# Kernel tuning notes

Measured on AMD Instinct MI355X. Metric: run time of the kernel, lower is better.

The kernel has to match this reference:

```python
import jax, jax.numpy as jnp
import numpy as np

N_NODES = 50000
N_EDGES = 625000
IN_DIM = 128
OUT_DIM = 128


def setup_inputs() -> dict:
    key = jax.random.key(0)
    ks = jax.random.split(key, 8)
    feats = jax.random.normal(ks[0], (N_NODES, IN_DIM), dtype=jnp.float32)
    src = jax.random.randint(ks[1], (N_EDGES,), 0, N_NODES, dtype=jnp.int64)
    dst = jax.random.randint(ks[2], (N_EDGES,), 0, N_NODES, dtype=jnp.int64)
    # nn.Linear default init: U(-1/sqrt(fan_in), 1/sqrt(fan_in))
    bf = 1.0 / np.sqrt(IN_DIM)
    W_f = jax.random.uniform(ks[3], (OUT_DIM, IN_DIM), jnp.float32, -bf, bf)
    b_f = jax.random.uniform(ks[4], (OUT_DIM,), jnp.float32, -bf, bf)
    bp = 1.0 / np.sqrt(OUT_DIM)
    W_phy = jax.random.uniform(ks[5], (OUT_DIM, OUT_DIM), jnp.float32, -bp, bp)
    b_phy = jax.random.uniform(ks[6], (OUT_DIM,), jnp.float32, -bp, bp)
    eps = jnp.zeros((1,), dtype=jnp.float32)  # init_eps = 0
    return {"feats": feats, "src": src, "dst": dst, "W_f": W_f, "b_f": b_f,
            "W_phy": W_phy, "b_phy": b_phy, "eps": eps}


def reference(feats, src, dst, W_f, b_f, W_phy, b_phy, eps):
    # mlp_f (num_mlps=1): linear + relu
    h = jax.nn.relu(feats @ W_f.T + b_f)              # [N, out_dim]
    # update_all(copy_u('h'), sum): sum messages h[src] at dst
    n = jax.ops.segment_sum(h[src], dst, num_segments=N_NODES)  # [N, out_dim]
    # faithful to source: h = 1 + eps * h + n
    h = 1.0 + eps * h + n
    # mlp_phy (num_mlps=1): linear + relu
    h = jax.nn.relu(h @ W_phy.T + b_phy)
    return h
```

## Files before the change

kernel.cpp:

```cpp
#include <hip/hip_runtime.h>

#define N_NODES 50000
#define N_EDGES 625000
#define DIM 128
#define RCAP 16
#define OCAP 64

typedef __bf16 bf16x8 __attribute__((ext_vector_type(8)));
typedef __bf16 bf16x4 __attribute__((ext_vector_type(4)));
typedef __bf16 bf16x2 __attribute__((ext_vector_type(2)));
typedef float f32x4 __attribute__((ext_vector_type(4)));

__device__ __forceinline__ float bflo(unsigned u) { return __uint_as_float(u << 16); }
__device__ __forceinline__ float bfhi(unsigned u) { return __uint_as_float(u & 0xffff0000u); }

__global__ __launch_bounds__(512) void gemm1_fill_k(
    const float* __restrict__ A_f32,
    const float* __restrict__ W,
    const float* __restrict__ bias,
    __bf16* __restrict__ out_bf16,
    const int* __restrict__ src,
    const int* __restrict__ dst,
    int* __restrict__ cnt9,
    int* __restrict__ bucket,
    int* __restrict__ obucket,
    const float* __restrict__ W_phy,
    __bf16* __restrict__ Wb,
    int gemm_blocks)
{
    const int t = threadIdx.x;

    if ((int)blockIdx.x >= gemm_blocks) {
        if ((int)blockIdx.x == gemm_blocks) {
            if (t < 16) {
                bf16x8 z = {};
                *(bf16x8*)&out_bf16[(size_t)N_NODES * DIM + t * 8] = z;
            }
            for (int i = t; i < 4096; i += 512) {
                float4 f = ((const float4*)W_phy)[i];
                bf16x4 pk = { (__bf16)f.x, (__bf16)f.y, (__bf16)f.z, (__bf16)f.w };
                *(bf16x4*)&Wb[i * 4] = pk;
            }
        }
        int xcd;
        asm volatile("s_getreg_b32 %0, hwreg(HW_REG_XCC_ID)" : "=s"(xcd));
        xcd &= 7;
        const int cb = xcd * N_NODES;

        int idx = ((int)blockIdx.x - gemm_blocks) * 512 + t;
        if (idx < N_EDGES / 8) {
            int4 sa = ((const int4*)src)[idx * 2];
            int4 sb = ((const int4*)src)[idx * 2 + 1];
            int4 da = ((const int4*)dst)[idx * 2];
            int4 db = ((const int4*)dst)[idx * 2 + 1];
            int p0 = atomicAdd(&cnt9[cb + da.x], 1);
            int p1 = atomicAdd(&cnt9[cb + da.y], 1);
            int p2 = atomicAdd(&cnt9[cb + da.z], 1);
            int p3 = atomicAdd(&cnt9[cb + da.w], 1);
            int p4 = atomicAdd(&cnt9[cb + db.x], 1);
            int p5 = atomicAdd(&cnt9[cb + db.y], 1);
            int p6 = atomicAdd(&cnt9[cb + db.z], 1);
            int p7 = atomicAdd(&cnt9[cb + db.w], 1);
            if (p0 < RCAP) bucket[((cb + da.x) << 4) + p0] = sa.x;
            else { int q = atomicAdd(&cnt9[8 * N_NODES + da.x], 1); obucket[(da.x << 6) + q] = sa.x; }
            if (p1 < RCAP) bucket[((cb + da.y) << 4) + p1] = sa.y;
            else { int q = atomicAdd(&cnt9[8 * N_NODES + da.y], 1); obucket[(da.y << 6) + q] = sa.y; }
            if (p2 < RCAP) bucket[((cb + da.z) << 4) + p2] = sa.z;
            else { int q = atomicAdd(&cnt9[8 * N_NODES + da.z], 1); obucket[(da.z << 6) + q] = sa.z; }
            if (p3 < RCAP) bucket[((cb + da.w) << 4) + p3] = sa.w;
            else { int q = atomicAdd(&cnt9[8 * N_NODES + da.w], 1); obucket[(da.w << 6) + q] = sa.w; }
            if (p4 < RCAP) bucket[((cb + db.x) << 4) + p4] = sb.x;
            else { int q = atomicAdd(&cnt9[8 * N_NODES + db.x], 1); obucket[(db.x << 6) + q] = sb.x; }
            if (p5 < RCAP) bucket[((cb + db.y) << 4) + p5] = sb.y;
            else { int q = atomicAdd(&cnt9[8 * N_NODES + db.y], 1); obucket[(db.y << 6) + q] = sb.y; }
            if (p6 < RCAP) bucket[((cb + db.z) << 4) + p6] = sb.z;
            else { int q = atomicAdd(&cnt9[8 * N_NODES + db.z], 1); obucket[(db.z << 6) + q] = sb.z; }
            if (p7 < RCAP) bucket[((cb + db.w) << 4) + p7] = sb.w;
            else { int q = atomicAdd(&cnt9[8 * N_NODES + db.w], 1); obucket[(db.w << 6) + q] = sb.w; }
        }
        return;
    }

    __shared__ __align__(16) __bf16 w_lds[128 * 136];

    for (int i = t; i < 4096; i += 512) {
        float4 f = ((const float4*)W)[i];
        int n = i >> 5;
        int k = (i & 31) << 2;
        bf16x4 pk = { (__bf16)f.x, (__bf16)f.y, (__bf16)f.z, (__bf16)f.w };
        *(bf16x4*)&w_lds[n * 136 + k] = pk;
    }
    __syncthreads();

    const int wave = t >> 6;
    const int lane = t & 63;
    const int q = lane >> 4;
    const int mr = lane & 15;

    const int m0 = blockIdx.x * 128 + wave * 16;
    int arow = m0 + mr;
    if (arow >= N_NODES) arow = N_NODES - 1;

    f32x4 acc[8] = {};

#pragma unroll
    for (int ks = 0; ks < 4; ++ks) {
        const int k0 = ks * 32 + q * 8;
        const float4* ap = (const float4*)&A_f32[(size_t)arow * DIM + k0];
        float4 a0 = ap[0], a1 = ap[1];
        bf16x8 af;
        af[0] = (__bf16)a0.x; af[1] = (__bf16)a0.y;
        af[2] = (__bf16)a0.z; af[3] = (__bf16)a0.w;
        af[4] = (__bf16)a1.x; af[5] = (__bf16)a1.y;
        af[6] = (__bf16)a1.z; af[7] = (__bf16)a1.w;
#pragma unroll
        for (int nt = 0; nt < 8; ++nt) {
            bf16x8 bfr = *(const bf16x8*)&w_lds[(nt * 16 + mr) * 136 + k0];
            acc[nt] = __builtin_amdgcn_mfma_f32_16x16x32_bf16(af, bfr, acc[nt], 0, 0, 0);
        }
    }

    __syncthreads();
    float* lds_f = (float*)w_lds;
    const int nb = blockIdx.x * 128;

#pragma unroll
    for (int half = 0; half < 2; ++half) {
        if ((wave >> 2) == half) {
            int lw = wave & 3;
#pragma unroll
            for (int nt = 0; nt < 8; ++nt)
#pragma unroll
                for (int r = 0; r < 4; ++r)
                    lds_f[(lw * 16 + q * 4 + r) * 132 + nt * 16 + mr] = acc[nt][r];
        }
        __syncthreads();
        for (int i = t; i < 2048; i += 512) {
            int lr = i >> 5;
            int cg = (i & 31) << 2;
            int grow = nb + half * 64 + lr;
            if (grow < N_NODES) {
                float4 v = *(const float4*)&lds_f[lr * 132 + cg];
                float4 b4 = *(const float4*)&bias[cg];
                bf16x4 o;
                o[0] = (__bf16)fmaxf(v.x + b4.x, 0.f);
                o[1] = (__bf16)fmaxf(v.y + b4.y, 0.f);
                o[2] = (__bf16)fmaxf(v.z + b4.z, 0.f);
                o[3] = (__bf16)fmaxf(v.w + b4.w, 0.f);
                *(bf16x4*)&out_bf16[(size_t)grow * DIM + cg] = o;
            }
        }
        __syncthreads();
    }
}

__global__ __launch_bounds__(512, 4) void agg_gemm2_k(
    const __bf16* __restrict__ h,
    const int* __restrict__ cnt9,
    const int* __restrict__ bucket,
    const int* __restrict__ obucket,
    const float* __restrict__ eps_p,
    const __bf16* __restrict__ Wb,
    const float* __restrict__ bias,
    float* __restrict__ out)
{
    __shared__ __align__(16) __bf16 lds[2 * 128 * 136];
    __shared__ __align__(16) int widx_all[8][200];
    __bf16* const w_lds = lds;
    __bf16* const a_lds = lds + 128 * 136;

    const int t = threadIdx.x;

    for (int i = t; i < 2048; i += 512) {
        int n = i >> 4;
        int kk = (i & 15) << 3;
        bf16x8 v = *(const bf16x8*)&Wb[n * DIM + kk];
        *(bf16x8*)&w_lds[n * 136 + kk] = v;
    }

    const int wave = t >> 6;
    const int lane = t & 63;
    const int ch = lane << 1;
    const int xq = lane >> 4;
    const int sj = lane & 15;
    const int rowbase = __builtin_amdgcn_readfirstlane(blockIdx.x * 128 + wave * 16);
    const float eps = eps_p[0];
    int* const widx = widx_all[wave];

    int ndv[2], cAv[2], cBv[2], rAv[2], rBv[2], ocv[2];
    unsigned svv[2];
    auto nload = [&](int sl, int ii) {
        const int node = rowbase + ii;
        const int nd = (node < N_NODES) ? node : (N_NODES - 1);
        ndv[sl] = nd;
        int ca = cnt9[xq * N_NODES + nd];
        int cb = cnt9[(xq + 4) * N_NODES + nd];
        cAv[sl] = (ca < RCAP) ? ca : RCAP;
        cBv[sl] = (cb < RCAP) ? cb : RCAP;
        rAv[sl] = bucket[((xq * N_NODES + nd) << 4) + sj];
        rBv[sl] = bucket[(((xq + 4) * N_NODES + nd) << 4) + sj];
        ocv[sl] = cnt9[8 * N_NODES + nd];
        svv[sl] = *(const unsigned*)&h[(size_t)nd * DIM + ch];
    };
    nload(0, 0);

#pragma unroll
    for (int i = 0; i < 16; ++i) {
        if (i < 15) nload((i + 1) & 1, i + 1);
        const int sl = i & 1;
        const int nd = ndv[sl];

        const unsigned long long mA = __ballot(sj < cAv[sl]);
        const unsigned long long mB = __ballot(sj < cBv[sl]);
        const unsigned long long below = (1ull << lane) - 1ull;
        const int tA = __popcll(mA);
        int deg = tA + __popcll(mB);
        if (sj < cAv[sl]) widx[__popcll(mA & below)] = rAv[sl];
        if (sj < cBv[sl]) widx[tA + __popcll(mB & below)] = rBv[sl];
        const int oc = ocv[sl];
        if (oc > 0) {
            if (lane < oc) widx[deg + lane] = obucket[(nd << 6) + lane];
            deg += oc;
        }
        if (lane < 8) widx[deg + lane] = N_NODES;

        float ax = 0.f, ay = 0.f;
        for (int e = 0; e < deg; e += 8) {
            int4 w0 = *(const int4*)&widx[e];
            int4 w1 = *(const int4*)&widx[e + 4];
            unsigned v0 = *(const unsigned*)&h[(size_t)w0.x * DIM + ch];
            unsigned v1 = *(const unsigned*)&h[(size_t)w0.y * DIM + ch];
            unsigned v2 = *(const unsigned*)&h[(size_t)w0.z * DIM + ch];
            unsigned v3 = *(const unsigned*)&h[(size_t)w0.w * DIM + ch];
            unsigned v4 = *(const unsigned*)&h[(size_t)w1.x * DIM + ch];
            unsigned v5 = *(const unsigned*)&h[(size_t)w1.y * DIM + ch];
            unsigned v6 = *(const unsigned*)&h[(size_t)w1.z * DIM + ch];
            unsigned v7 = *(const unsigned*)&h[(size_t)w1.w * DIM + ch];
            ax += (bflo(v0) + bflo(v1)) + (bflo(v2) + bflo(v3))
                + (bflo(v4) + bflo(v5)) + (bflo(v6) + bflo(v7));
            ay += (bfhi(v0) + bfhi(v1)) + (bfhi(v2) + bfhi(v3))
                + (bfhi(v4) + bfhi(v5)) + (bfhi(v6) + bfhi(v7));
        }
        ax = 1.0f + eps * bflo(svv[sl]) + ax;
        ay = 1.0f + eps * bfhi(svv[sl]) + ay;
        bf16x2 o; o[0] = (__bf16)ax; o[1] = (__bf16)ay;
        *(bf16x2*)&a_lds[(wave * 16 + i) * 136 + ch] = o;
    }

    __syncthreads();

    const int q = lane >> 4;
    const int mr = lane & 15;

    f32x4 acc[8] = {};

#pragma unroll
    for (int ks = 0; ks < 4; ++ks) {
        const int k0 = ks * 32 + q * 8;
        bf16x8 af = *(const bf16x8*)&a_lds[(wave * 16 + mr) * 136 + k0];
#pragma unroll
        for (int nt = 0; nt < 8; ++nt) {
            bf16x8 bfr = *(const bf16x8*)&w_lds[(nt * 16 + mr) * 136 + k0];
            acc[nt] = __builtin_amdgcn_mfma_f32_16x16x32_bf16(af, bfr, acc[nt], 0, 0, 0);
        }
    }

    __syncthreads();
    float* lds_f = (float*)lds;
    const int nb = blockIdx.x * 128;

#pragma unroll
    for (int half = 0; half < 2; ++half) {
        if ((wave >> 2) == half) {
            int lw = wave & 3;
#pragma unroll
            for (int nt = 0; nt < 8; ++nt)
#pragma unroll
                for (int r = 0; r < 4; ++r)
                    lds_f[(lw * 16 + q * 4 + r) * 132 + nt * 16 + mr] = acc[nt][r];
        }
        __syncthreads();
        for (int i2 = t; i2 < 2048; i2 += 512) {
            int lr = i2 >> 5;
            int cg = (i2 & 31) << 2;
            int grow = nb + half * 64 + lr;
            if (grow < N_NODES) {
                float4 v = *(const float4*)&lds_f[lr * 132 + cg];
                float4 b4 = *(const float4*)&bias[cg];
                v.x = fmaxf(v.x + b4.x, 0.f);
                v.y = fmaxf(v.y + b4.y, 0.f);
                v.z = fmaxf(v.z + b4.z, 0.f);
                v.w = fmaxf(v.w + b4.w, 0.f);
                *(float4*)&out[(size_t)grow * DIM + cg] = v;
            }
        }
        __syncthreads();
    }
}

extern "C" void kernel_launch(void* const* d_in, const int* in_sizes, int n_in,
                              void* d_out, int out_size, void* d_ws, size_t ws_size,
                              hipStream_t stream) {
    const float* feats = (const float*)d_in[0];
    const int*   src   = (const int*)d_in[1];
    const int*   dst   = (const int*)d_in[2];
    const float* W_f   = (const float*)d_in[3];
    const float* b_f   = (const float*)d_in[4];
    const float* W_phy = (const float*)d_in[5];
    const float* b_phy = (const float*)d_in[6];
    const float* eps   = (const float*)d_in[7];
    float* out = (float*)d_out;

    const size_t HN = (size_t)(N_NODES + 1) * DIM;
    __bf16* h    = (__bf16*)d_ws;
    int* bucket  = (int*)(h + HN);
    int* obucket = bucket + (size_t)8 * N_NODES * RCAP;
    int* cnt9    = obucket + (size_t)N_NODES * OCAP;
    __bf16* Wb   = (__bf16*)(cnt9 + (size_t)9 * N_NODES);

    const int gblocks = (N_NODES + 127) / 128;
    const int fblocks = (N_EDGES / 8 + 511) / 512;

    hipMemsetAsync(cnt9, 0, (size_t)9 * N_NODES * sizeof(int), stream);

    gemm1_fill_k<<<gblocks + fblocks, 512, 0, stream>>>(
        feats, W_f, b_f, h, src, dst, cnt9, bucket, obucket, W_phy, Wb, gblocks);

    agg_gemm2_k<<<gblocks, 512, 0, stream>>>(
        h, cnt9, bucket, obucket, eps, Wb, b_phy, out);
}
```

Before: 154.7 us.

## Split fused GEMM1/fill kernel and store bucket source indices as 16-bit

The fused kernel that ran the first GEMM and the edge bucketing as different block ranges is split into two separate launches, gemm1_k and fill_k. The bucket array now stores source node ids as unsigned short instead of int, which halves its footprint and the bytes written and gathered for bucket entries. The 16-bit ids fit only because N_NODES is below 65536. Splitting the kernel gives up the concurrent execution of the compute-bound GEMM and the atomic-bound fill, and adds a launch.

```diff
diff --git a/kernel.cpp b/kernel.cpp
--- a/kernel.cpp
+++ b/kernel.cpp
@@ -14,73 +14,75 @@
 __device__ __forceinline__ float bflo(unsigned u) { return __uint_as_float(u << 16); }
 __device__ __forceinline__ float bfhi(unsigned u) { return __uint_as_float(u & 0xffff0000u); }
 
-__global__ __launch_bounds__(512) void gemm1_fill_k(
+__global__ __launch_bounds__(512) void fill_k(
+    const int* __restrict__ src,
+    const int* __restrict__ dst,
+    int* __restrict__ cnt9,
+    unsigned short* __restrict__ bucket,
+    int* __restrict__ obucket,
+    const float* __restrict__ W_phy,
+    __bf16* __restrict__ Wb,
+    __bf16* __restrict__ out_bf16)
+{
+    const int t = threadIdx.x;
+
+    if (blockIdx.x == 0) {
+        if (t < 16) {
+            bf16x8 z = {};
+            *(bf16x8*)&out_bf16[(size_t)N_NODES * DIM + t * 8] = z;
+        }
+        for (int i = t; i < 4096; i += 512) {
+            float4 f = ((const float4*)W_phy)[i];
+            bf16x4 pk = { (__bf16)f.x, (__bf16)f.y, (__bf16)f.z, (__bf16)f.w };
+            *(bf16x4*)&Wb[i * 4] = pk;
+        }
+    }
+
+    int xcd;
+    asm volatile("s_getreg_b32 %0, hwreg(HW_REG_XCC_ID)" : "=s"(xcd));
+    xcd &= 7;
+    const int cb = xcd * N_NODES;
+
+    const int idx = (int)blockIdx.x * 512 + t;
+    if (idx < N_EDGES / 8) {
+        int4 sa = ((const int4*)src)[idx * 2];
+        int4 sb = ((const int4*)src)[idx * 2 + 1];
+        int4 da = ((const int4*)dst)[idx * 2];
+        int4 db = ((const int4*)dst)[idx * 2 + 1];
+        int p0 = atomicAdd(&cnt9[cb + da.x], 1);
+        int p1 = atomicAdd(&cnt9[cb + da.y], 1);
+        int p2 = atomicAdd(&cnt9[cb + da.z], 1);
+        int p3 = atomicAdd(&cnt9[cb + da.w], 1);
+        int p4 = atomicAdd(&cnt9[cb + db.x], 1);
+        int p5 = atomicAdd(&cnt9[cb + db.y], 1);
+        int p6 = atomicAdd(&cnt9[cb + db.z], 1);
+        int p7 = atomicAdd(&cnt9[cb + db.w], 1);
+        if (p0 < RCAP) bucket[((cb + da.x) << 4) + p0] = (unsigned short)sa.x;
+        else { int q = atomicAdd(&cnt9[8 * N_NODES + da.x], 1); obucket[(da.x << 6) + q] = sa.x; }
+        if (p1 < RCAP) bucket[((cb + da.y) << 4) + p1] = (unsigned short)sa.y;
+        else { int q = atomicAdd(&cnt9[8 * N_NODES + da.y], 1); obucket[(da.y << 6) + q] = sa.y; }
+        if (p2 < RCAP) bucket[((cb + da.z) << 4) + p2] = (unsigned short)sa.z;
+        else { int q = atomicAdd(&cnt9[8 * N_NODES + da.z], 1); obucket[(da.z << 6) + q] = sa.z; }
+        if (p3 < RCAP) bucket[((cb + da.w) << 4) + p3] = (unsigned short)sa.w;
+        else { int q = atomicAdd(&cnt9[8 * N_NODES + da.w], 1); obucket[(da.w << 6) + q] = sa.w; }
+        if (p4 < RCAP) bucket[((cb + db.x) << 4) + p4] = (unsigned short)sb.x;
+        else { int q = atomicAdd(&cnt9[8 * N_NODES + db.x], 1); obucket[(db.x << 6) + q] = sb.x; }
+        if (p5 < RCAP) bucket[((cb + db.y) << 4) + p5] = (unsigned short)sb.y;
+        else { int q = atomicAdd(&cnt9[8 * N_NODES + db.y], 1); obucket[(db.y << 6) + q] = sb.y; }
+        if (p6 < RCAP) bucket[((cb + db.z) << 4) + p6] = (unsigned short)sb.z;
+        else { int q = atomicAdd(&cnt9[8 * N_NODES + db.z], 1); obucket[(db.z << 6) + q] = sb.z; }
+        if (p7 < RCAP) bucket[((cb + db.w) << 4) + p7] = (unsigned short)sb.w;
+        else { int q = atomicAdd(&cnt9[8 * N_NODES + db.w], 1); obucket[(db.w << 6) + q] = sb.w; }
+    }
+}
+
+__global__ __launch_bounds__(512) void gemm1_k(
     const float* __restrict__ A_f32,
     const float* __restrict__ W,
     const float* __restrict__ bias,
-    __bf16* __restrict__ out_bf16,
-    const int* __restrict__ src,
-    const int* __restrict__ dst,
-    int* __restrict__ cnt9,
-    int* __restrict__ bucket,
-    int* __restrict__ obucket,
-    const float* __restrict__ W_phy,
-    __bf16* __restrict__ Wb,
-    int gemm_blocks)
+    __bf16* __restrict__ out_bf16)
 {
     const int t = threadIdx.x;
-
-    if ((int)blockIdx.x >= gemm_blocks) {
-        if ((int)blockIdx.x == gemm_blocks) {
-            if (t < 16) {
-                bf16x8 z = {};
-                *(bf16x8*)&out_bf16[(size_t)N_NODES * DIM + t * 8] = z;
-            }
-            for (int i = t; i < 4096; i += 512) {
-                float4 f = ((const float4*)W_phy)[i];
-                bf16x4 pk = { (__bf16)f.x, (__bf16)f.y, (__bf16)f.z, (__bf16)f.w };
-                *(bf16x4*)&Wb[i * 4] = pk;
-            }
-        }
-        int xcd;
-        asm volatile("s_getreg_b32 %0, hwreg(HW_REG_XCC_ID)" : "=s"(xcd));
-        xcd &= 7;
-        const int cb = xcd * N_NODES;
-
-        int idx = ((int)blockIdx.x - gemm_blocks) * 512 + t;
-        if (idx < N_EDGES / 8) {
-            int4 sa = ((const int4*)src)[idx * 2];
-            int4 sb = ((const int4*)src)[idx * 2 + 1];
-            int4 da = ((const int4*)dst)[idx * 2];
-            int4 db = ((const int4*)dst)[idx * 2 + 1];
-            int p0 = atomicAdd(&cnt9[cb + da.x], 1);
-            int p1 = atomicAdd(&cnt9[cb + da.y], 1);
-            int p2 = atomicAdd(&cnt9[cb + da.z], 1);
-            int p3 = atomicAdd(&cnt9[cb + da.w], 1);
-            int p4 = atomicAdd(&cnt9[cb + db.x], 1);
-            int p5 = atomicAdd(&cnt9[cb + db.y], 1);
-            int p6 = atomicAdd(&cnt9[cb + db.z], 1);
-            int p7 = atomicAdd(&cnt9[cb + db.w], 1);
-            if (p0 < RCAP) bucket[((cb + da.x) << 4) + p0] = sa.x;
-            else { int q = atomicAdd(&cnt9[8 * N_NODES + da.x], 1); obucket[(da.x << 6) + q] = sa.x; }
-            if (p1 < RCAP) bucket[((cb + da.y) << 4) + p1] = sa.y;
-            else { int q = atomicAdd(&cnt9[8 * N_NODES + da.y], 1); obucket[(da.y << 6) + q] = sa.y; }
-            if (p2 < RCAP) bucket[((cb + da.z) << 4) + p2] = sa.z;
-            else { int q = atomicAdd(&cnt9[8 * N_NODES + da.z], 1); obucket[(da.z << 6) + q] = sa.z; }
-            if (p3 < RCAP) bucket[((cb + da.w) << 4) + p3] = sa.w;
-            else { int q = atomicAdd(&cnt9[8 * N_NODES + da.w], 1); obucket[(da.w << 6) + q] = sa.w; }
-            if (p4 < RCAP) bucket[((cb + db.x) << 4) + p4] = sb.x;
-            else { int q = atomicAdd(&cnt9[8 * N_NODES + db.x], 1); obucket[(db.x << 6) + q] = sb.x; }
-            if (p5 < RCAP) bucket[((cb + db.y) << 4) + p5] = sb.y;
-            else { int q = atomicAdd(&cnt9[8 * N_NODES + db.y], 1); obucket[(db.y << 6) + q] = sb.y; }
-            if (p6 < RCAP) bucket[((cb + db.z) << 4) + p6] = sb.z;
-            else { int q = atomicAdd(&cnt9[8 * N_NODES + db.z], 1); obucket[(db.z << 6) + q] = sb.z; }
-            if (p7 < RCAP) bucket[((cb + db.w) << 4) + p7] = sb.w;
-            else { int q = atomicAdd(&cnt9[8 * N_NODES + db.w], 1); obucket[(db.w << 6) + q] = sb.w; }
-        }
-        return;
-    }
-
     __shared__ __align__(16) __bf16 w_lds[128 * 136];
 
     for (int i = t; i < 4096; i += 512) {
@@ -157,7 +159,7 @@
 __global__ __launch_bounds__(512, 4) void agg_gemm2_k(
     const __bf16* __restrict__ h,
     const int* __restrict__ cnt9,
-    const int* __restrict__ bucket,
+    const unsigned short* __restrict__ bucket,
     const int* __restrict__ obucket,
     const float* __restrict__ eps_p,
     const __bf16* __restrict__ Wb,
@@ -197,8 +199,8 @@
         int cb = cnt9[(xq + 4) * N_NODES + nd];
         cAv[sl] = (ca < RCAP) ? ca : RCAP;
         cBv[sl] = (cb < RCAP) ? cb : RCAP;
-        rAv[sl] = bucket[((xq * N_NODES + nd) << 4) + sj];
-        rBv[sl] = bucket[(((xq + 4) * N_NODES + nd) << 4) + sj];
+        rAv[sl] = (int)bucket[((xq * N_NODES + nd) << 4) + sj];
+        rBv[sl] = (int)bucket[(((xq + 4) * N_NODES + nd) << 4) + sj];
         ocv[sl] = cnt9[8 * N_NODES + nd];
         svv[sl] = *(const unsigned*)&h[(size_t)nd * DIM + ch];
     };
@@ -313,8 +315,8 @@
 
     const size_t HN = (size_t)(N_NODES + 1) * DIM;
     __bf16* h    = (__bf16*)d_ws;
-    int* bucket  = (int*)(h + HN);
-    int* obucket = bucket + (size_t)8 * N_NODES * RCAP;
+    unsigned short* bucket = (unsigned short*)(h + HN);
+    int* obucket = (int*)(bucket + (size_t)8 * N_NODES * RCAP);
     int* cnt9    = obucket + (size_t)N_NODES * OCAP;
     __bf16* Wb   = (__bf16*)(cnt9 + (size_t)9 * N_NODES);
 
@@ -323,8 +325,10 @@
 
     hipMemsetAsync(cnt9, 0, (size_t)9 * N_NODES * sizeof(int), stream);
 
-    gemm1_fill_k<<<gblocks + fblocks, 512, 0, stream>>>(
-        feats, W_f, b_f, h, src, dst, cnt9, bucket, obucket, W_phy, Wb, gblocks);
+    gemm1_k<<<gblocks, 512, 0, stream>>>(feats, W_f, b_f, h);
+
+    fill_k<<<fblocks, 512, 0, stream>>>(
+        src, dst, cnt9, bucket, obucket, W_phy, Wb, h);
 
     agg_gemm2_k<<<gblocks, 512, 0, stream>>>(
         h, cnt9, bucket, obucket, eps, Wb, b_phy, out);
```

After: 160.5 us. +3.8%, slower.
